# Optimization experiments

Hardware: AMD Instinct MI355X
Metric: run time of the kernel (lower is better)

## Reference

```python
import jax, jax.numpy as jnp
import numpy as np

N, E, H, C, G = 10000, 20000, 12, 768, 64  # nodes, edges, heads, per-head dim, graphs
NEG_SLOPE = 0.2


def _gat_layer(x, W, a_src, a_dst, b, src, dst):
    # x: [N, 768], W: [768, H*C], a_src/a_dst: [H, C], b: [C]
    h = (x @ W).reshape(-1, H, C)                      # [N, H, C]
    s = jnp.einsum('nhc,hc->nh', h, a_src)             # alpha_src per node
    d = jnp.einsum('nhc,hc->nh', h, a_dst)             # alpha_dst per node
    e = jax.nn.leaky_relu(s[src] + d[dst], NEG_SLOPE)  # [Etot, H]
    # segment softmax over incoming edges of each destination node
    m = jax.lax.stop_gradient(jax.ops.segment_max(e, dst, num_segments=N))
    ex = jnp.exp(e - m[dst])
    den = jax.ops.segment_sum(ex, dst, num_segments=N)
    alpha = ex / (den[dst] + 1e-16)                    # [Etot, H]
    out = jax.ops.segment_sum(h[src] * alpha[:, :, None], dst, num_segments=N)
    return out.mean(axis=1) + b                        # concat=False -> head mean, [N, C]


def setup_inputs() -> dict:
    key = jax.random.key(0)
    ks = jax.random.split(key, 16)
    sc = 0.02
    f32 = jnp.float32
    return {
        'x': jax.random.normal(ks[0], (N, 768), f32),
        'edge_index': jax.random.randint(ks[1], (2, E), 0, N),
        'batch': jnp.sort(jax.random.randint(ks[2], (N,), 0, G)),
        'W1': (jax.random.normal(ks[3], (768, H * C), f32) * sc),
        'a_src1': (jax.random.normal(ks[4], (H, C), f32) * sc),
        'a_dst1': (jax.random.normal(ks[5], (H, C), f32) * sc),
        'b1': jnp.zeros((C,), f32),
        'W2': (jax.random.normal(ks[6], (768, H * C), f32) * sc),
        'a_src2': (jax.random.normal(ks[7], (H, C), f32) * sc),
        'a_dst2': (jax.random.normal(ks[8], (H, C), f32) * sc),
        'b2': jnp.zeros((C,), f32),
        'mlp_w1': (jax.random.normal(ks[9], (768, 128), f32) * sc),
        'mlp_b1': jnp.zeros((128,), f32),
        'mlp_w2': (jax.random.normal(ks[10], (128, 4), f32) * sc),
        'mlp_b2': jnp.zeros((4,), f32),
    }


def reference(x, edge_index, batch, W1, a_src1, a_dst1, b1, W2, a_src2, a_dst2, b2,
              mlp_w1, mlp_b1, mlp_w2, mlp_b2):
    loops = jnp.arange(N)                               # GATConv add_self_loops=True
    src = jnp.concatenate([edge_index[0], loops])
    dst = jnp.concatenate([edge_index[1], loops])
    h = _gat_layer(x, W1, a_src1, a_dst1, b1, src, dst)
    h = _gat_layer(h, W2, a_src2, a_dst2, b2, src, dst)
    # scatter_mean over graph assignment
    ssum = jax.ops.segment_sum(h, batch, num_segments=G)
    cnt = jax.ops.segment_sum(jnp.ones((N,), h.dtype), batch, num_segments=G)
    g = ssum / jnp.maximum(cnt, 1.0)[:, None]           # [G, 768]
    z = jax.nn.relu(g @ mlp_w1 + mlp_b1)
    return z @ mlp_w2 + mlp_b2                          # [G, 4] logits
```

## Files before the change

### kernel.cpp

```cpp
#include <hip/hip_runtime.h>
#include <stdint.h>

typedef unsigned short u16;
typedef unsigned int   u32;

#define NNODES 10000
#define NEDGES 20000
#define ETOT   30000
#define NHEADS 12
#define CDIM   768
#define FDIM   768
#define KDIM   9216
#define NGRAPH 64
#define MPAD   10240
#define NEG_SLOPE 0.2f
#define DMAX   32
#define NPLANE 144

typedef __attribute__((ext_vector_type(8))) short short8;
typedef __attribute__((ext_vector_type(4))) float f32x4;

__device__ __forceinline__ u16 f32_bf16(float f) {
  u32 u = __float_as_uint(f);
  u = (u + 0x7FFFu + ((u >> 16) & 1u)) >> 16;
  return (u16)u;
}
__device__ __forceinline__ float bf16_f32(u16 v) {
  return __uint_as_float(((u32)v) << 16);
}

__global__ void k_count(const int* __restrict__ dste, int* __restrict__ counts) {
  int e = blockIdx.x * blockDim.x + threadIdx.x;
  if (e >= ETOT) return;
  int dst;
  if (e < NEDGES) dst = dste[e]; else dst = e - NEDGES;
  atomicAdd(&counts[dst], 1);
}

__global__ void k_scan(const int* __restrict__ counts, int* __restrict__ offs) {
  __shared__ int part[256];
  int t = threadIdx.x;
  const int chunk = 40;
  int beg = t * chunk;
  int end = beg + chunk; if (end > NNODES) end = NNODES;
  int s = 0;
  for (int i = beg; i < end && i < NNODES; i++) s += counts[i];
  part[t] = s;
  __syncthreads();
  for (int d = 1; d < 256; d <<= 1) {
    int v = (t >= d) ? part[t - d] : 0;
    __syncthreads();
    part[t] += v;
    __syncthreads();
  }
  int base = (t == 0) ? 0 : part[t - 1];
  for (int i = beg; i < end && i < NNODES; i++) { offs[i] = base; base += counts[i]; }
  if (t == 255) offs[NNODES] = base;
}

__global__ void k_seed(const int* __restrict__ offs, int* __restrict__ cursor) {
  int n = blockIdx.x * blockDim.x + threadIdx.x;
  if (n < NNODES) cursor[n] = offs[n];
}

__global__ void k_scatter(const int* __restrict__ dste, int* __restrict__ cursor,
                          int* __restrict__ elist) {
  int e = blockIdx.x * blockDim.x + threadIdx.x;
  if (e >= ETOT) return;
  int dst;
  if (e < NEDGES) dst = dste[e]; else dst = e - NEDGES;
  int pos = atomicAdd(&cursor[dst], 1);
  elist[pos] = e;
}

__global__ void k_U(const float* __restrict__ W, const float* __restrict__ a_src,
                    const float* __restrict__ a_dst, float* __restrict__ Ut) {
  int k = blockIdx.x;
  int t = threadIdx.x, w = t >> 6, l = t & 63;
  const float* Wrow = W + (size_t)k * KDIM;
#pragma unroll
  for (int q = 0; q < 6; q++) {
    int o = w * 6 + q;
    int h = (o < 12) ? o : o - 12;
    const float* av = (o < 12) ? (a_src + h * CDIM) : (a_dst + h * CDIM);
    const float* wr = Wrow + h * CDIM;
    float p = 0.f;
    for (int c = l; c < CDIM; c += 64) p += wr[c] * av[c];
#pragma unroll
    for (int d = 32; d > 0; d >>= 1) p += __shfl_down(p, d, 64);
    if (l == 0) Ut[o * FDIM + k] = p;
  }
}

__global__ void k_sd(const float* __restrict__ xin, const float* __restrict__ Ut,
                     float* __restrict__ sd) {
  __shared__ float UtS[24 * FDIM];
  int t = threadIdx.x, w = t >> 6, l = t & 63;
  const float4* U4 = (const float4*)Ut;
  float4* S4 = (float4*)UtS;
  for (int i = t; i < 24 * FDIM / 4; i += 256) S4[i] = U4[i];
  __syncthreads();
#pragma unroll
  for (int rep = 0; rep < 5; rep++) {
    int n = blockIdx.x * 20 + w * 5 + rep;
    if (n >= NNODES) continue;
    const float* xr = xin + (size_t)n * FDIM;
    float4 x0 = *(const float4*)(xr + 4 * l);
    float4 x1 = *(const float4*)(xr + 4 * l + 256);
    float4 x2 = *(const float4*)(xr + 4 * l + 512);
#pragma unroll
    for (int o = 0; o < 24; o++) {
      const float4* up = (const float4*)(UtS + o * FDIM + 4 * l);
      float4 u0 = up[0];
      float4 u1 = up[64];
      float4 u2 = up[128];
      float a = x0.x * u0.x + x0.y * u0.y + x0.z * u0.z + x0.w * u0.w
              + x1.x * u1.x + x1.y * u1.y + x1.z * u1.z + x1.w * u1.w
              + x2.x * u2.x + x2.y * u2.y + x2.z * u2.z + x2.w * u2.w;
#pragma unroll
      for (int d = 32; d > 0; d >>= 1) a += __shfl_xor(a, d, 64);
      if (l == 0) sd[n * 24 + o] = a;
    }
  }
}

__global__ void k_trans2(const float* __restrict__ W, u16* __restrict__ Bt2) {
  int kb = blockIdx.x * 32, jt = blockIdx.y * 32;
  int tx = threadIdx.x, ty = threadIdx.y;
  __shared__ float tile[32][33];
  int h0 = jt / 768, c0 = jt - h0 * 768;
  int plane = (h0 * 768 + kb) >> 6;
#pragma unroll
  for (int r = 0; r < 4; r++)
    tile[ty + 8 * r][tx] = W[(size_t)(kb + ty + 8 * r) * KDIM + jt + tx];
  __syncthreads();
#pragma unroll
  for (int r = 0; r < 4; r++)
    Bt2[(size_t)plane * (768 * 64) + (size_t)(c0 + ty + 8 * r) * 64 + ((kb + tx) & 63)]
        = f32_bf16(tile[tx][ty + 8 * r]);
}

__global__ void k_zpad(u16* __restrict__ y) {
  int idx = blockIdx.x * 256 + threadIdx.x;
  if (idx >= NPLANE * (MPAD - NNODES) * 8) return;
  int e = idx * 8;
  int plane = e / ((MPAD - NNODES) * 64);
  int rem = e - plane * ((MPAD - NNODES) * 64);
  u16* p = y + (size_t)plane * (MPAD * 64) + (size_t)NNODES * 64 + rem;
  *(short8*)p = (short8){0, 0, 0, 0, 0, 0, 0, 0};
}

__global__ void k_agg(const float* __restrict__ xin, const int* __restrict__ ei,
                      const int* __restrict__ offs, const int* __restrict__ elist,
                      const float* __restrict__ sd, u16* __restrict__ y) {
  int t = threadIdx.x, w = t >> 6, l = t & 63;
  int n = blockIdx.x * 4 + w;
  __shared__ int   srcsS[4][DMAX];
  __shared__ float alphS[4][NHEADS * DMAX];
  if (n >= NNODES) return;
  int* srcs = srcsS[w];
  float* alph = alphS[w];
  int beg = offs[n];
  int deg = offs[n + 1] - beg;
  if (deg > DMAX) deg = DMAX;
  if (l < deg) {
    int e = elist[beg + l];
    srcs[l] = (e < NEDGES) ? ei[e] : e - NEDGES;
  }
  __builtin_amdgcn_wave_barrier();
  for (int p = l; p < deg * NHEADS; p += 64) {
    int i = p / NHEADS, h = p - i * NHEADS;
    float v = sd[srcs[i] * 24 + h] + sd[n * 24 + 12 + h];
    v = (v > 0.f) ? v : NEG_SLOPE * v;
    alph[h * DMAX + i] = v;
  }
  __builtin_amdgcn_wave_barrier();
  if (l < NHEADS) {
    float m = -1e30f;
    for (int i = 0; i < deg; i++) m = fmaxf(m, alph[l * DMAX + i]);
    float s = 0.f;
    for (int i = 0; i < deg; i++) {
      float ex = expf(alph[l * DMAX + i] - m);
      alph[l * DMAX + i] = ex;
      s += ex;
    }
    float inv = 1.f / (s + 1e-16f);
    for (int i = 0; i < deg; i++) alph[l * DMAX + i] *= inv;
  }
  __builtin_amdgcn_wave_barrier();
  int lg = l >> 4, lo16 = l & 15;
#pragma unroll
  for (int pass = 0; pass < 3; pass++) {
    float4 acc12[NHEADS];
#pragma unroll
    for (int h = 0; h < NHEADS; h++) acc12[h] = make_float4(0.f, 0.f, 0.f, 0.f);
    for (int i = 0; i < deg; i++) {
      float4 xs = *(const float4*)(xin + (size_t)srcs[i] * FDIM + pass * 256 + 4 * l);
#pragma unroll
      for (int h = 0; h < NHEADS; h++) {
        float a = alph[h * DMAX + i];
        acc12[h].x += a * xs.x;
        acc12[h].y += a * xs.y;
        acc12[h].z += a * xs.z;
        acc12[h].w += a * xs.w;
      }
    }
#pragma unroll
    for (int h = 0; h < NHEADS; h++) {
      ushort4 pv;
      pv.x = f32_bf16(acc12[h].x);
      pv.y = f32_bf16(acc12[h].y);
      pv.z = f32_bf16(acc12[h].z);
      pv.w = f32_bf16(acc12[h].w);
      int plane = h * 12 + pass * 4 + lg;
      *(ushort4*)(y + (size_t)plane * (MPAD * 64) + (size_t)n * 64 + 4 * lo16) = pv;
    }
  }
}

#define GLL16(G, L) __builtin_amdgcn_global_load_lds( \
  (const __attribute__((address_space(1))) void*)(G), \
  (__attribute__((address_space(3))) void*)(L), 16, 0, 0)

__global__ __launch_bounds__(512, 4) void k_gemm2(const u16* __restrict__ A,
    const u16* __restrict__ B, float* __restrict__ C0, float* __restrict__ C1) {
  __shared__ __align__(16) u16 As[2][256 * 32];
  __shared__ __align__(16) u16 Bs[2][128 * 32];
  int t = threadIdx.x;
  int w = t >> 6, l = t & 63;
  int bid = blockIdx.x;
  int xcd = bid & 7, j = bid >> 3;
  int p = j / 12, rem = j - p * 12;
  int ks = rem / 6, cx = rem - ks * 6;
  int row0 = (xcd * 5 + p) * 256, col0 = cx * 128;
  int K0b = ks * NPLANE;
  int wr = w >> 1, wc = w & 1;
  int lr = l & 15, lg = l >> 4;
  int koff = lg * 16;
  int swzr = (lr & 3) << 4;
  int rb = t >> 2;
  int csw = ((t & 3) ^ (rb & 3)) * 8;

  f32x4 acc[4][4] = {};
  short8 alo[2], ahi[2], blo[2], bhi[2];

  auto stA = [&](int buf, int h, int K0) {
    int kt2 = K0 >> 1, hf = (K0 & 1) * 32;
    const u16* g = A + (size_t)kt2 * (MPAD * 64)
                     + (size_t)(row0 + h * 128 + rb) * 64 + hf + csw;
    GLL16(g, (u16*)&As[buf][0] + h * 4096 + (w << 9));
  };
  auto stB = [&](int buf, int K0) {
    int kt2 = K0 >> 1, hf = (K0 & 1) * 32;
    const u16* g = B + (size_t)kt2 * (768 * 64)
                     + (size_t)(col0 + rb) * 64 + hf + csw;
    GLL16(g, (u16*)&Bs[buf][0] + (w << 9));
  };
  auto ldA = [&](int buf, short8* d, int mo) {
#pragma unroll
    for (int m = 0; m < 2; m++) {
      int row = wr * 64 + (mo + m) * 16 + lr;
      d[m] = *(const short8*)((const char*)&As[buf][0] + row * 64 + (koff ^ swzr));
    }
  };
  auto ldB = [&](int buf, short8* d, int no) {
#pragma unroll
    for (int n = 0; n < 2; n++) {
      int row = wc * 64 + (no + n) * 16 + lr;
      d[n] = *(const short8*)((const char*)&Bs[buf][0] + row * 64 + (koff ^ swzr));
    }
  };
  auto mm4 = [&](short8* aa, short8* bb, int mo, int no) {
    __builtin_amdgcn_s_setprio(1);
#pragma unroll
    for (int m = 0; m < 2; m++)
#pragma unroll
      for (int n = 0; n < 2; n++)
        acc[mo + m][no + n] = __builtin_amdgcn_mfma_f32_16x16x32_bf16(
            aa[m], bb[n], acc[mo + m][no + n], 0, 0, 0);
    __builtin_amdgcn_s_setprio(0);
  };

  stB(0, K0b); stA(0, 0, K0b); stA(0, 1, K0b);
  stB(1, K0b + 1); stA(1, 0, K0b + 1);
  asm volatile("s_waitcnt vmcnt(2)" ::: "memory");
  __builtin_amdgcn_s_barrier();

  const int NIT = NPLANE;
  for (int s = 0; s < NIT; s++) {
    int P = s & 1;
    int K0 = K0b + s;
    ldA(P, alo, 0); ldB(P, blo, 0);
    __builtin_amdgcn_s_barrier();
    mm4(alo, blo, 0, 0);
    __builtin_amdgcn_s_barrier();
    ldB(P, bhi, 2);
    if (s + 1 < NIT) stA(P ^ 1, 1, K0 + 1);
    __builtin_amdgcn_s_barrier();
    mm4(alo, bhi, 0, 2);
    __builtin_amdgcn_s_barrier();
    ldA(P, ahi, 2);
    if (s + 2 < NIT) stB(P, K0 + 2);
    __builtin_amdgcn_s_barrier();
    mm4(ahi, bhi, 2, 2);
    __builtin_amdgcn_s_barrier();
    if (s + 2 < NIT) stA(P, 0, K0 + 2);
    __builtin_amdgcn_s_barrier();
    mm4(ahi, blo, 2, 0);
    if (s < NIT - 1) {
      if (s <= NIT - 3) asm volatile("s_waitcnt vmcnt(2)" ::: "memory");
      else              asm volatile("s_waitcnt vmcnt(0)" ::: "memory");
    }
    __builtin_amdgcn_s_barrier();
  }

  float* Cd = ks ? C1 : C0;
#pragma unroll
  for (int m = 0; m < 4; m++)
#pragma unroll
    for (int n = 0; n < 4; n++) {
      int col = col0 + wc * 64 + n * 16 + lr;
#pragma unroll
      for (int r = 0; r < 4; r++) {
        int row = row0 + wr * 64 + m * 16 + lg * 4 + r;
        if (row < NNODES)
          Cd[(size_t)row * FDIM + col] = acc[m][n][r];
      }
    }
}

__global__ void k_red(const float* __restrict__ p1, const float* __restrict__ bias,
                      float* __restrict__ io) {
  int e = (blockIdx.x * 256 + threadIdx.x) * 4;
  float4 a = *(const float4*)(io + e);
  float4 b = *(const float4*)(p1 + e);
  float4 bv = *(const float4*)(bias + (e % FDIM));
  const float sc = 1.f / 12.f;
  float4 o;
  o.x = (a.x + b.x) * sc + bv.x;
  o.y = (a.y + b.y) * sc + bv.y;
  o.z = (a.z + b.z) * sc + bv.z;
  o.w = (a.w + b.w) * sc + bv.w;
  *(float4*)(io + e) = o;
}

__global__ void k_pool(const float* __restrict__ h2, const int* __restrict__ batch,
                       float* __restrict__ g) {
  int gi = blockIdx.x;
  int c = blockIdx.y * 256 + threadIdx.x;
  int lo = 0, hi = NNODES;
  while (lo < hi) { int mid = (lo + hi) >> 1; if (batch[mid] < gi) lo = mid + 1; else hi = mid; }
  int start = lo;
  lo = start; hi = NNODES;
  while (lo < hi) { int mid = (lo + hi) >> 1; if (batch[mid] < gi + 1) lo = mid + 1; else hi = mid; }
  int end = lo;
  int cnt = end - start; if (cnt < 1) cnt = 1;
  float inv = 1.f / (float)cnt;
  float s = 0.f;
  for (int n = start; n < end; n++) s += h2[(size_t)n * FDIM + c];
  g[gi * FDIM + c] = s * inv;
}

__global__ void k_mlp(const float* __restrict__ g, const float* __restrict__ w1,
                      const float* __restrict__ b1, const float* __restrict__ w2,
                      const float* __restrict__ b2, float* __restrict__ out) {
  int gi = blockIdx.x;
  int t = threadIdx.x;
  __shared__ float gs[FDIM];
  __shared__ float zs[128];
  for (int i = t; i < FDIM; i += 128) gs[i] = g[gi * FDIM + i];
  __syncthreads();
  float a = b1[t];
  for (int k = 0; k < FDIM; k++) a += gs[k] * w1[k * 128 + t];
  zs[t] = (a > 0.f) ? a : 0.f;
  __syncthreads();
  if (t < 4) {
    float o = b2[t];
    for (int i = 0; i < 128; i++) o += zs[i] * w2[i * 4 + t];
    out[gi * 4 + t] = o;
  }
}

extern "C" void kernel_launch(void* const* d_in, const int* in_sizes, int n_in,
                              void* d_out, int out_size, void* d_ws, size_t ws_size,
                              hipStream_t stream) {
  const float* x    = (const float*)d_in[0];
  const int*   ei   = (const int*)d_in[1];
  const int*   batch= (const int*)d_in[2];
  const float* W1   = (const float*)d_in[3];
  const float* as1  = (const float*)d_in[4];
  const float* ad1  = (const float*)d_in[5];
  const float* b1   = (const float*)d_in[6];
  const float* W2   = (const float*)d_in[7];
  const float* as2  = (const float*)d_in[8];
  const float* ad2  = (const float*)d_in[9];
  const float* b2   = (const float*)d_in[10];
  const float* mw1  = (const float*)d_in[11];
  const float* mb1  = (const float*)d_in[12];
  const float* mw2  = (const float*)d_in[13];
  const float* mb2  = (const float*)d_in[14];
  float* out = (float*)d_out;
  (void)in_sizes; (void)n_in; (void)out_size; (void)ws_size;

  char* wsb = (char*)d_ws;
  size_t off = 0;
  auto alloc = [&](size_t bytes) -> void* {
    void* p = wsb + off;
    off += (bytes + 255) & ~(size_t)255;
    return p;
  };
  u16*  y      = (u16*)alloc((size_t)MPAD * KDIM * 2);
  u16*  Bt2    = (u16*)alloc((size_t)FDIM * KDIM * 2);
  float* h1    = (float*)alloc((size_t)NNODES * FDIM * 4);
  float* h2    = (float*)alloc((size_t)NNODES * FDIM * 4);
  float* sd    = (float*)alloc((size_t)NNODES * 24 * 4);
  float* Ut    = (float*)alloc((size_t)FDIM * 24 * 4);
  int*  counts = (int*)alloc((size_t)NNODES * 4);
  int*  offs   = (int*)alloc((size_t)(NNODES + 1) * 4);
  int*  cursor = (int*)alloc((size_t)NNODES * 4);
  int*  elist  = (int*)alloc((size_t)ETOT * 4);
  float* gbuf  = (float*)alloc((size_t)NGRAPH * FDIM * 4);

  hipMemsetAsync(counts, 0, NNODES * 4, stream);
  k_zpad<<<(NPLANE * (MPAD - NNODES) * 8 + 255) / 256, 256, 0, stream>>>(y);
  k_count<<<(ETOT + 255) / 256, 256, 0, stream>>>(ei + NEDGES, counts);
  k_scan<<<1, 256, 0, stream>>>(counts, offs);
  k_seed<<<(NNODES + 255) / 256, 256, 0, stream>>>(offs, cursor);
  k_scatter<<<(ETOT + 255) / 256, 256, 0, stream>>>(ei + NEDGES, cursor, elist);

  for (int layer = 0; layer < 2; layer++) {
    const float* xin  = layer ? h1  : x;
    const float* W    = layer ? W2  : W1;
    const float* asrc = layer ? as2 : as1;
    const float* adst = layer ? ad2 : ad1;
    const float* bb   = layer ? b2  : b1;
    float* hout       = layer ? h2  : h1;
    float* cpart      = layer ? h1  : h2;

    k_U<<<FDIM, 256, 0, stream>>>(W, asrc, adst, Ut);
    k_sd<<<(NNODES + 19) / 20, 256, 0, stream>>>(xin, Ut, sd);
    k_trans2<<<dim3(FDIM / 32, KDIM / 32), dim3(32, 8), 0, stream>>>(W, Bt2);
    k_agg<<<(NNODES + 3) / 4, 256, 0, stream>>>(xin, ei, offs, elist, sd, y);
    k_gemm2<<<480, 512, 0, stream>>>(y, Bt2, hout, cpart);
    k_red<<<NNODES * FDIM / 1024, 256, 0, stream>>>(cpart, bb, hout);
  }

  k_pool<<<dim3(NGRAPH, 3), 256, 0, stream>>>(h2, batch, gbuf);
  k_mlp<<<NGRAPH, 128, 0, stream>>>(gbuf, mw1, mb1, mw2, mb2, out);
}
```

Measured before the change: 901.1 us.

## Restructure GEMM to 4 waves with 128x64 per-wave tiles and 64-wide K stages

Rewrites the bf16 MFMA GEMM kernel to use 256 threads (4 waves) per block instead of 512. Each wave now computes a 128x64 output tile, and each iteration stages a whole 64-wide K plane into a single LDS buffer with an 8-way XOR swizzle. The aim is more register-level reuse per wave and fewer barriers per K step. In exchange it drops the double-buffered, interleaved load/compute pipeline, so global-to-LDS loads are no longer overlapped with MFMA work, and the larger accumulator raises register pressure.

```diff
diff --git a/kernel.cpp b/kernel.cpp
--- a/kernel.cpp
+++ b/kernel.cpp
@@ -222,10 +222,10 @@
   (const __attribute__((address_space(1))) void*)(G), \
   (__attribute__((address_space(3))) void*)(L), 16, 0, 0)
 
-__global__ __launch_bounds__(512, 4) void k_gemm2(const u16* __restrict__ A,
+__global__ __launch_bounds__(256, 2) void k_gemm2(const u16* __restrict__ A,
     const u16* __restrict__ B, float* __restrict__ C0, float* __restrict__ C1) {
-  __shared__ __align__(16) u16 As[2][256 * 32];
-  __shared__ __align__(16) u16 Bs[2][128 * 32];
+  __shared__ __align__(16) u16 As[256 * 64];
+  __shared__ __align__(16) u16 Bs[128 * 64];
   int t = threadIdx.x;
   int w = t >> 6, l = t & 63;
   int bid = blockIdx.x;
@@ -233,96 +233,71 @@
   int p = j / 12, rem = j - p * 12;
   int ks = rem / 6, cx = rem - ks * 6;
   int row0 = (xcd * 5 + p) * 256, col0 = cx * 128;
-  int K0b = ks * NPLANE;
+  int K0b = ks * (NPLANE / 2);
   int wr = w >> 1, wc = w & 1;
   int lr = l & 15, lg = l >> 4;
-  int koff = lg * 16;
-  int swzr = (lr & 3) << 4;
-  int rb = t >> 2;
-  int csw = ((t & 3) ^ (rb & 3)) * 8;
-
-  f32x4 acc[4][4] = {};
-  short8 alo[2], ahi[2], blo[2], bhi[2];
-
-  auto stA = [&](int buf, int h, int K0) {
-    int kt2 = K0 >> 1, hf = (K0 & 1) * 32;
-    const u16* g = A + (size_t)kt2 * (MPAD * 64)
-                     + (size_t)(row0 + h * 128 + rb) * 64 + hf + csw;
-    GLL16(g, (u16*)&As[buf][0] + h * 4096 + (w << 9));
+  int swzr = (lr & 7) << 4;
+
+  f32x4 acc[8][4] = {};
+
+  auto stage = [&](int pl) {
+#pragma unroll
+    for (int i = 0; i < 8; i++) {
+      int idx = i * 256 + t;
+      int rb = idx >> 3, cc = idx & 7;
+      const u16* g = A + (size_t)pl * (MPAD * 64)
+                       + (size_t)(row0 + rb) * 64 + ((cc ^ (rb & 7)) * 8);
+      GLL16(g, (u16*)As + idx * 8);
+    }
+#pragma unroll
+    for (int i = 0; i < 4; i++) {
+      int idx = i * 256 + t;
+      int rb = idx >> 3, cc = idx & 7;
+      const u16* g = B + (size_t)pl * (768 * 64)
+                       + (size_t)(col0 + rb) * 64 + ((cc ^ (rb & 7)) * 8);
+      GLL16(g, (u16*)Bs + idx * 8);
+    }
   };
-  auto stB = [&](int buf, int K0) {
-    int kt2 = K0 >> 1, hf = (K0 & 1) * 32;
-    const u16* g = B + (size_t)kt2 * (768 * 64)
-                     + (size_t)(col0 + rb) * 64 + hf + csw;
-    GLL16(g, (u16*)&Bs[buf][0] + (w << 9));
-  };
-  auto ldA = [&](int buf, short8* d, int mo) {
-#pragma unroll
-    for (int m = 0; m < 2; m++) {
-      int row = wr * 64 + (mo + m) * 16 + lr;
-      d[m] = *(const short8*)((const char*)&As[buf][0] + row * 64 + (koff ^ swzr));
-    }
-  };
-  auto ldB = [&](int buf, short8* d, int no) {
-#pragma unroll
-    for (int n = 0; n < 2; n++) {
-      int row = wc * 64 + (no + n) * 16 + lr;
-      d[n] = *(const short8*)((const char*)&Bs[buf][0] + row * 64 + (koff ^ swzr));
-    }
-  };
-  auto mm4 = [&](short8* aa, short8* bb, int mo, int no) {
-    __builtin_amdgcn_s_setprio(1);
-#pragma unroll
-    for (int m = 0; m < 2; m++)
-#pragma unroll
-      for (int n = 0; n < 2; n++)
-        acc[mo + m][no + n] = __builtin_amdgcn_mfma_f32_16x16x32_bf16(
-            aa[m], bb[n], acc[mo + m][no + n], 0, 0, 0);
-    __builtin_amdgcn_s_setprio(0);
-  };
-
-  stB(0, K0b); stA(0, 0, K0b); stA(0, 1, K0b);
-  stB(1, K0b + 1); stA(1, 0, K0b + 1);
-  asm volatile("s_waitcnt vmcnt(2)" ::: "memory");
-  __builtin_amdgcn_s_barrier();
-
-  const int NIT = NPLANE;
+
+  const int NIT = NPLANE / 2;
   for (int s = 0; s < NIT; s++) {
-    int P = s & 1;
-    int K0 = K0b + s;
-    ldA(P, alo, 0); ldB(P, blo, 0);
-    __builtin_amdgcn_s_barrier();
-    mm4(alo, blo, 0, 0);
-    __builtin_amdgcn_s_barrier();
-    ldB(P, bhi, 2);
-    if (s + 1 < NIT) stA(P ^ 1, 1, K0 + 1);
-    __builtin_amdgcn_s_barrier();
-    mm4(alo, bhi, 0, 2);
-    __builtin_amdgcn_s_barrier();
-    ldA(P, ahi, 2);
-    if (s + 2 < NIT) stB(P, K0 + 2);
-    __builtin_amdgcn_s_barrier();
-    mm4(ahi, bhi, 2, 2);
-    __builtin_amdgcn_s_barrier();
-    if (s + 2 < NIT) stA(P, 0, K0 + 2);
-    __builtin_amdgcn_s_barrier();
-    mm4(ahi, blo, 2, 0);
-    if (s < NIT - 1) {
-      if (s <= NIT - 3) asm volatile("s_waitcnt vmcnt(2)" ::: "memory");
-      else              asm volatile("s_waitcnt vmcnt(0)" ::: "memory");
-    }
-    __builtin_amdgcn_s_barrier();
+    stage(K0b + s);
+    __syncthreads();
+    short8 a[8], b[4];
+#pragma unroll
+    for (int kc = 0; kc < 2; kc++) {
+      int koff = (kc * 64 + lg * 16);
+#pragma unroll
+      for (int m = 0; m < 8; m++) {
+        int row = wr * 128 + m * 16 + lr;
+        a[m] = *(const short8*)((const char*)As + row * 128 + (koff ^ swzr));
+      }
+#pragma unroll
+      for (int n = 0; n < 4; n++) {
+        int row = wc * 64 + n * 16 + lr;
+        b[n] = *(const short8*)((const char*)Bs + row * 128 + (koff ^ swzr));
+      }
+      __builtin_amdgcn_s_setprio(1);
+#pragma unroll
+      for (int m = 0; m < 8; m++)
+#pragma unroll
+        for (int n = 0; n < 4; n++)
+          acc[m][n] = __builtin_amdgcn_mfma_f32_16x16x32_bf16(
+              a[m], b[n], acc[m][n], 0, 0, 0);
+      __builtin_amdgcn_s_setprio(0);
+    }
+    __syncthreads();
   }
 
   float* Cd = ks ? C1 : C0;
 #pragma unroll
-  for (int m = 0; m < 4; m++)
+  for (int m = 0; m < 8; m++)
 #pragma unroll
     for (int n = 0; n < 4; n++) {
       int col = col0 + wc * 64 + n * 16 + lr;
 #pragma unroll
       for (int r = 0; r < 4; r++) {
-        int row = row0 + wr * 64 + m * 16 + lg * 4 + r;
+        int row = row0 + wr * 128 + m * 16 + lg * 4 + r;
         if (row < NNODES)
           Cd[(size_t)row * FDIM + col] = acc[m][n][r];
       }
@@ -441,7 +416,7 @@
     k_sd<<<(NNODES + 19) / 20, 256, 0, stream>>>(xin, Ut, sd);
     k_trans2<<<dim3(FDIM / 32, KDIM / 32), dim3(32, 8), 0, stream>>>(W, Bt2);
     k_agg<<<(NNODES + 3) / 4, 256, 0, stream>>>(xin, ei, offs, elist, sd, y);
-    k_gemm2<<<480, 512, 0, stream>>>(y, Bt2, hout, cpart);
+    k_gemm2<<<480, 256, 0, stream>>>(y, Bt2, hout, cpart);
     k_red<<<NNODES * FDIM / 1024, 256, 0, stream>>>(cpart, bb, hout);
   }
 
```

After: 793.3 us. 1.14x faster.
